# Kernel tuning notes

Hardware: AMD Instinct MI355X
Metric: run time of the kernel (lower is better)

Reference implementation:

```python
import jax, jax.numpy as jnp
import numpy as np

D_MODEL = 768
N_HEAD = 12
D_FF = 3072
SEQ = 2048
BSZ = 4
EPS = 1e-5


def _linear_params(key, d_in, d_out):
    k1, k2 = jax.random.split(key)
    bound = 1.0 / np.sqrt(d_in)
    W = jax.random.uniform(k1, (d_in, d_out), jnp.float32, -bound, bound)
    b = jax.random.uniform(k2, (d_out,), jnp.float32, -bound, bound)
    return W, b


def setup_inputs() -> dict:
    key = jax.random.key(0)
    ks = jax.random.split(key, 8)
    src = jax.random.normal(ks[0], (SEQ, BSZ, D_MODEL), jnp.float32)
    Wq, bq = _linear_params(ks[1], D_MODEL, D_MODEL)
    Wk, bk = _linear_params(ks[2], D_MODEL, D_MODEL)
    Wv, bv = _linear_params(ks[3], D_MODEL, D_MODEL)
    Wo, bo = _linear_params(ks[4], D_MODEL, D_MODEL)
    W1, b1 = _linear_params(ks[5], D_MODEL, D_FF)
    W2, b2 = _linear_params(ks[6], D_FF, D_MODEL)
    g1 = jnp.ones((D_MODEL,), jnp.float32)
    be1 = jnp.zeros((D_MODEL,), jnp.float32)
    g2 = jnp.ones((D_MODEL,), jnp.float32)
    be2 = jnp.zeros((D_MODEL,), jnp.float32)
    return dict(src=src, Wq=Wq, bq=bq, Wk=Wk, bk=bk, Wv=Wv, bv=bv,
                Wo=Wo, bo=bo, W1=W1, b1=b1, W2=W2, b2=b2,
                g1=g1, be1=be1, g2=g2, be2=be2)


def _layer_norm(x, g, b):
    mu = jnp.mean(x, axis=-1, keepdims=True)
    var = jnp.mean(jnp.square(x - mu), axis=-1, keepdims=True)
    return (x - mu) * jax.lax.rsqrt(var + EPS) * g + b


def reference(src, Wq, bq, Wk, bk, Wv, bv, Wo, bo, W1, b1, W2, b2, g1, be1, g2, be2):
    L, B, D = src.shape
    H = N_HEAD
    hd = D // H
    # in-projection: (L,B,D) -> (B*H, L, hd)
    def split_heads(x):
        return x.reshape(L, B * H, hd).transpose(1, 0, 2)
    q = split_heads(src @ Wq + bq)
    k = split_heads(src @ Wk + bk)
    v = split_heads(src @ Wv + bv)
    # NOTE: original code applies NO 1/sqrt(head_dim) scaling
    scores = jnp.einsum('bqd,bkd->bqk', q, k)  # (B*H, L, L)
    attn = jax.nn.softmax(scores, axis=-1)
    attn_out = jnp.einsum('bqk,bkd->bqd', attn, v)  # (B*H, L, hd)
    # out-projection
    attn_out = attn_out.transpose(1, 0, 2).reshape(L, B, D)
    src2 = attn_out @ Wo + bo
    x = _layer_norm(src + src2, g1, be1)
    ff = jax.nn.gelu(x @ W1 + b1, approximate=False) @ W2 + b2
    return _layer_norm(x + ff, g2, be2)
```

## Files before the change

kernel.cpp:

```cpp
#include <hip/hip_runtime.h>
#include <math.h>

#define D_MODEL 768
#define N_HEAD  12
#define HD      64
#define D_FF    3072
#define SEQ     2048
#define BSZ     4
#define NROWS   (SEQ * BSZ)

typedef unsigned short u16;
typedef __attribute__((ext_vector_type(8))) short short8;
typedef __attribute__((ext_vector_type(4))) float float4v;

enum { FLAG_GELU = 1 };

__device__ __forceinline__ float gelu_exact(float x) {
    return 0.5f * x * (1.0f + erff(x * 0.70710678118654752440f));
}
__device__ __forceinline__ u16 f2b(float f) {
    unsigned u = __builtin_bit_cast(unsigned, f);
    return (u16)((u + 0x7fffu + ((u >> 16) & 1u)) >> 16);
}
__device__ __forceinline__ float b2f(u16 x) {
    return __builtin_bit_cast(float, (unsigned)x << 16);
}
__device__ __forceinline__ void gll16(const u16* g, u16* l) {
    __builtin_amdgcn_global_load_lds(
        (const __attribute__((address_space(1))) unsigned*)g,
        (__attribute__((address_space(3))) unsigned*)l, 16, 0, 0);
}

__global__ __launch_bounds__(256) void gemm_bt(
    const u16* __restrict__ A, int lda,
    const u16* __restrict__ Bt, int ldb,
    const float* __restrict__ bias,
    const float* __restrict__ residf, const u16* __restrict__ residb, int ldr,
    float* __restrict__ Cf, u16* __restrict__ Cb, int ldc,
    int K, int flags)
{
    __shared__ u16 Ab[128 * 32];
    __shared__ u16 Bb[128 * 32];

    const int tid  = threadIdx.x;
    const int lane = tid & 63, wv = tid >> 6;
    const int row0 = blockIdx.x * 128, col0 = blockIdx.y * 128;
    const int mw = (wv & 1) * 64, nw = (wv >> 1) * 64;
    const int fr = lane & 15, fk = (lane >> 4) * 8;

    float4v acc[4][4];
    #pragma unroll
    for (int i = 0; i < 4; ++i)
        #pragma unroll
        for (int j = 0; j < 4; ++j)
            acc[i][j] = float4v{0.f, 0.f, 0.f, 0.f};

    for (int k0 = 0; k0 < K; k0 += 32) {
        __syncthreads();
        #pragma unroll
        for (int i = 0; i < 2; ++i) {
            const int cid = i * 256 + wv * 64 + lane;
            const int r = cid >> 2, ch = (cid & 3) * 8;
            gll16(A  + (size_t)(row0 + r) * lda + k0 + ch, Ab + (size_t)cid * 8);
            gll16(Bt + (size_t)(col0 + r) * ldb + k0 + ch, Bb + (size_t)cid * 8);
        }
        __syncthreads();

        short8 af[4], bfr[4];
        #pragma unroll
        for (int t = 0; t < 4; ++t) {
            af[t]  = *(const short8*)&Ab[(mw + t * 16 + fr) * 32 + fk];
            bfr[t] = *(const short8*)&Bb[(nw + t * 16 + fr) * 32 + fk];
        }
        #pragma unroll
        for (int mt = 0; mt < 4; ++mt)
            #pragma unroll
            for (int nt = 0; nt < 4; ++nt)
                acc[mt][nt] = __builtin_amdgcn_mfma_f32_16x16x32_bf16(
                    af[mt], bfr[nt], acc[mt][nt], 0, 0, 0);
    }

    #pragma unroll
    for (int mt = 0; mt < 4; ++mt)
        #pragma unroll
        for (int nt = 0; nt < 4; ++nt)
            #pragma unroll
            for (int r = 0; r < 4; ++r) {
                const int row = row0 + mw + mt * 16 + (lane >> 4) * 4 + r;
                const int col = col0 + nw + nt * 16 + fr;
                float v = acc[mt][nt][r];
                if (bias)              v += bias[col];
                if (flags & FLAG_GELU) v = gelu_exact(v);
                if (residf)            v += residf[(size_t)row * ldr + col];
                if (residb)            v += b2f(residb[(size_t)row * ldr + col]);
                if (Cf) Cf[(size_t)row * ldc + col] = v;
                if (Cb) Cb[(size_t)row * ldc + col] = f2b(v);
            }
}

__global__ __launch_bounds__(256) void vt_kernel(
    const u16* __restrict__ qkv, u16* __restrict__ vt)
{
    __shared__ u16 t[64][72];
    const int tid = threadIdx.x;
    const int bh = blockIdx.y, b = bh / N_HEAD, h = bh % N_HEAD;
    const int l0 = blockIdx.x * 64;
    #pragma unroll
    for (int p = 0; p < 2; ++p) {
        const int idx = p * 256 + tid;
        const int lr = idx >> 3, c8 = (idx & 7) * 8;
        *(short8*)&t[lr][c8] = *(const short8*)
            &qkv[((size_t)(l0 + lr) * BSZ + b) * 2304 + 1536 + h * 64 + c8];
    }
    __syncthreads();
    #pragma unroll
    for (int p = 0; p < 2; ++p) {
        const int idx = p * 256 + tid;
        const int dr = idx >> 3, l8 = (idx & 7) * 8;
        short8 vv;
        #pragma unroll
        for (int j = 0; j < 8; ++j) vv[j] = (short)t[l8 + j][dr];
        *(short8*)&vt[((size_t)(bh * 64 + dr)) * SEQ + l0 + l8] = vv;
    }
}

__global__ __launch_bounds__(256) void attn_kernel(
    const u16* __restrict__ qkv,
    const u16* __restrict__ vt,
    u16* __restrict__ o)
{
    __shared__ u16 Kt[64 * 64];
    __shared__ u16 Vt[64 * 64];
    __shared__ u16 PQ[128 * 72];

    const int tid  = threadIdx.x;
    const int lane = tid & 63, wv = tid >> 6;
    const int fr = lane & 15, hi = lane >> 4;
    const int bh = blockIdx.y, b = bh / N_HEAD, h = bh % N_HEAD;
    const int q0 = blockIdx.x * 128;

    #pragma unroll
    for (int i = 0; i < 4; ++i) {
        const int cid = i * 256 + wv * 64 + lane;
        const int r = cid >> 3, c = cid & 7;
        gll16(qkv + ((size_t)(q0 + r) * BSZ + b) * 2304 + h * 64 + ((c ^ (r & 7)) * 8),
              PQ + (size_t)cid * 8);
    }
    __syncthreads();
    short8 qf[2][2];
    #pragma unroll
    for (int mt = 0; mt < 2; ++mt) {
        const int row = wv * 32 + mt * 16 + fr;
        #pragma unroll
        for (int kb = 0; kb < 2; ++kb)
            qf[mt][kb] = *(const short8*)&PQ[row * 64 + (((kb << 2) + hi) ^ (fr & 7)) * 8];
    }

    const short8 ones = {(short)0x3F80, (short)0x3F80, (short)0x3F80, (short)0x3F80,
                         (short)0x3F80, (short)0x3F80, (short)0x3F80, (short)0x3F80};
    float4v oacc[2][4], ls[2];
    #pragma unroll
    for (int mt = 0; mt < 2; ++mt) {
        ls[mt] = float4v{0.f, 0.f, 0.f, 0.f};
        #pragma unroll
        for (int nt = 0; nt < 4; ++nt) oacc[mt][nt] = float4v{0.f, 0.f, 0.f, 0.f};
    }

    for (int kt = 0; kt < SEQ; kt += 64) {
        __syncthreads();
        #pragma unroll
        for (int i = 0; i < 2; ++i) {
            const int cid = i * 256 + wv * 64 + lane;
            const int r = cid >> 3, c = cid & 7;
            const int cs = (c ^ (r & 7)) * 8;
            gll16(qkv + ((size_t)(kt + r) * BSZ + b) * 2304 + 768 + h * 64 + cs,
                  Kt + (size_t)cid * 8);
            gll16(vt + (size_t)(bh * 64 + r) * SEQ + kt + cs,
                  Vt + (size_t)cid * 8);
        }
        __syncthreads();

        float4v s[2][4];
        #pragma unroll
        for (int mt = 0; mt < 2; ++mt)
            #pragma unroll
            for (int nt = 0; nt < 4; ++nt) s[mt][nt] = float4v{0.f, 0.f, 0.f, 0.f};
        #pragma unroll
        for (int kb = 0; kb < 2; ++kb) {
            short8 kfr[4];
            #pragma unroll
            for (int nt = 0; nt < 4; ++nt)
                kfr[nt] = *(const short8*)&Kt[(nt * 16 + fr) * 64 + (((kb << 2) + hi) ^ (fr & 7)) * 8];
            #pragma unroll
            for (int mt = 0; mt < 2; ++mt)
                #pragma unroll
                for (int nt = 0; nt < 4; ++nt)
                    s[mt][nt] = __builtin_amdgcn_mfma_f32_16x16x32_bf16(
                        qf[mt][kb], kfr[nt], s[mt][nt], 0, 0, 0);
        }

        #pragma unroll
        for (int mt = 0; mt < 2; ++mt)
            #pragma unroll
            for (int nt = 0; nt < 4; ++nt)
                #pragma unroll
                for (int r = 0; r < 4; ++r)
                    PQ[(wv * 32 + mt * 16 + hi * 4 + r) * 72 + nt * 16 + fr]
                        = f2b(__expf(s[mt][nt][r] - 16.0f));
        __syncthreads();

        #pragma unroll
        for (int kb = 0; kb < 2; ++kb) {
            short8 pf[2], vfr[4];
            #pragma unroll
            for (int mt = 0; mt < 2; ++mt)
                pf[mt] = *(const short8*)&PQ[(wv * 32 + mt * 16 + fr) * 72 + kb * 32 + hi * 8];
            #pragma unroll
            for (int nt = 0; nt < 4; ++nt)
                vfr[nt] = *(const short8*)&Vt[(nt * 16 + fr) * 64 + (((kb << 2) + hi) ^ (fr & 7)) * 8];
            #pragma unroll
            for (int mt = 0; mt < 2; ++mt) {
                ls[mt] = __builtin_amdgcn_mfma_f32_16x16x32_bf16(pf[mt], ones, ls[mt], 0, 0, 0);
                #pragma unroll
                for (int nt = 0; nt < 4; ++nt)
                    oacc[mt][nt] = __builtin_amdgcn_mfma_f32_16x16x32_bf16(
                        pf[mt], vfr[nt], oacc[mt][nt], 0, 0, 0);
            }
        }
    }

    #pragma unroll
    for (int mt = 0; mt < 2; ++mt)
        #pragma unroll
        for (int r = 0; r < 4; ++r) {
            const int qr = wv * 32 + mt * 16 + hi * 4 + r;
            const float linv = 1.0f / ls[mt][r];
            #pragma unroll
            for (int nt = 0; nt < 4; ++nt)
                o[((size_t)(q0 + qr) * BSZ + b) * D_MODEL + h * 64 + nt * 16 + fr]
                    = f2b(oacc[mt][nt][r] * linv);
        }
}

__global__ __launch_bounds__(256) void ln_kernel(
    const float* __restrict__ x, float* __restrict__ outf, u16* __restrict__ outb,
    const float* __restrict__ g, const float* __restrict__ be)
{
    const int row = blockIdx.x;
    const int tid = threadIdx.x;
    const float* xr = x + (size_t)row * D_MODEL;
    float v[3];
    float s = 0.0f, sq = 0.0f;
    #pragma unroll
    for (int j = 0; j < 3; ++j) {
        v[j] = xr[tid + 256 * j];
        s  += v[j];
        sq += v[j] * v[j];
    }
    #pragma unroll
    for (int off = 32; off > 0; off >>= 1) {
        s  += __shfl_down(s, off);
        sq += __shfl_down(sq, off);
    }
    __shared__ float ws_[8], wq_[8];
    if ((tid & 63) == 0) { ws_[tid >> 6] = s; wq_[tid >> 6] = sq; }
    __syncthreads();
    if (tid == 0) {
        float S = 0.0f, Q = 0.0f;
        #pragma unroll
        for (int w = 0; w < 4; ++w) { S += ws_[w]; Q += wq_[w]; }
        ws_[4] = S; wq_[4] = Q;
    }
    __syncthreads();
    const float mu   = ws_[4] * (1.0f / D_MODEL);
    const float var  = wq_[4] * (1.0f / D_MODEL) - mu * mu;
    const float rstd = rsqrtf(var + 1e-5f);
    #pragma unroll
    for (int j = 0; j < 3; ++j) {
        const int c = tid + 256 * j;
        const float y = (v[j] - mu) * rstd * g[c] + be[c];
        if (outf) outf[(size_t)row * D_MODEL + c] = y;
        if (outb) outb[(size_t)row * D_MODEL + c] = f2b(y);
    }
}

__global__ __launch_bounds__(256) void transpose_bf(
    const float* __restrict__ in, u16* __restrict__ out, int R, int Cn)
{
    __shared__ float t[32][33];
    const int c0 = blockIdx.x * 32, r0 = blockIdx.y * 32;
    const int tx = threadIdx.x & 31, ty = threadIdx.x >> 5;
    #pragma unroll
    for (int i = 0; i < 4; ++i)
        t[ty + i * 8][tx] = in[(size_t)(r0 + ty + i * 8) * Cn + c0 + tx];
    __syncthreads();
    #pragma unroll
    for (int i = 0; i < 4; ++i)
        out[(size_t)(c0 + ty + i * 8) * R + r0 + tx] = f2b(t[tx][ty + i * 8]);
}

__global__ __launch_bounds__(256) void conv_bf(
    const float* __restrict__ in, u16* __restrict__ out, int n4)
{
    const int i = blockIdx.x * 256 + threadIdx.x;
    if (i < n4) {
        const float4 vv = ((const float4*)in)[i];
        uint2 pk;
        pk.x = (unsigned)f2b(vv.x) | ((unsigned)f2b(vv.y) << 16);
        pk.y = (unsigned)f2b(vv.z) | ((unsigned)f2b(vv.w) << 16);
        ((uint2*)out)[i] = pk;
    }
}

__global__ __launch_bounds__(256) void pack_bias(
    const float* __restrict__ bq, const float* __restrict__ bk,
    const float* __restrict__ bv, float* __restrict__ dst)
{
    const int i = blockIdx.x * 256 + threadIdx.x;
    if (i < 2304)
        dst[i] = (i < 768) ? bq[i] : (i < 1536) ? bk[i - 768] : bv[i - 1536];
}

extern "C" void kernel_launch(void* const* d_in, const int* in_sizes, int n_in,
                              void* d_out, int out_size, void* d_ws, size_t ws_size,
                              hipStream_t stream)
{
    (void)in_sizes; (void)n_in; (void)out_size; (void)ws_size;
    const float* src = (const float*)d_in[0];
    const float* Wq  = (const float*)d_in[1];
    const float* bq  = (const float*)d_in[2];
    const float* Wk  = (const float*)d_in[3];
    const float* bk  = (const float*)d_in[4];
    const float* Wv  = (const float*)d_in[5];
    const float* bv  = (const float*)d_in[6];
    const float* Wo  = (const float*)d_in[7];
    const float* bo  = (const float*)d_in[8];
    const float* W1  = (const float*)d_in[9];
    const float* b1  = (const float*)d_in[10];
    const float* W2  = (const float*)d_in[11];
    const float* b2  = (const float*)d_in[12];
    const float* g1  = (const float*)d_in[13];
    const float* be1 = (const float*)d_in[14];
    const float* g2  = (const float*)d_in[15];
    const float* be2 = (const float*)d_in[16];
    float* out = (float*)d_out;

    char* w = (char*)d_ws;
    u16* WqkvT = (u16*)w; w += (size_t)2304 * 768 * 2;
    u16* WoT   = (u16*)w; w += (size_t)768 * 768 * 2;
    u16* W1T   = (u16*)w; w += (size_t)D_FF * 768 * 2;
    u16* W2T   = (u16*)w; w += (size_t)768 * D_FF * 2;
    float* bqkv = (float*)w; w += 2304 * 4 + 64;
    char* A0 = w; w += (size_t)NROWS * 768 * 2;
    char* A1 = w; w += (size_t)NROWS * 2304 * 2;
    char* A2 = w; w += (size_t)NROWS * 768 * 2;
    u16*   srcb  = (u16*)A0;
    u16*   vtb   = (u16*)A0;
    u16*   qkvb  = (u16*)A1;
    float* sum   = (float*)A1;
    u16*   attnb = (u16*)A2;
    u16*   x1b   = (u16*)A2;
    u16*   hb    = (u16*)A0;

    const dim3 blk(256);

    transpose_bf<<<dim3(24, 24), blk, 0, stream>>>(Wq, WqkvT,                 768, 768);
    transpose_bf<<<dim3(24, 24), blk, 0, stream>>>(Wk, WqkvT + 768 * 768,     768, 768);
    transpose_bf<<<dim3(24, 24), blk, 0, stream>>>(Wv, WqkvT + 2 * 768 * 768, 768, 768);
    transpose_bf<<<dim3(24, 24), blk, 0, stream>>>(Wo, WoT, 768, 768);
    transpose_bf<<<dim3(96, 24), blk, 0, stream>>>(W1, W1T, 768, 3072);
    transpose_bf<<<dim3(24, 96), blk, 0, stream>>>(W2, W2T, 3072, 768);
    pack_bias<<<dim3(9), blk, 0, stream>>>(bq, bk, bv, bqkv);
    conv_bf<<<dim3(NROWS * 768 / 4 / 256), blk, 0, stream>>>(src, srcb, NROWS * 768 / 4);

    gemm_bt<<<dim3(64, 18), blk, 0, stream>>>(srcb, 768, WqkvT, 768, bqkv,
        nullptr, nullptr, 0, nullptr, qkvb, 2304, 768, 0);

    vt_kernel<<<dim3(32, 48), blk, 0, stream>>>(qkvb, vtb);
    attn_kernel<<<dim3(SEQ / 128, BSZ * N_HEAD), blk, 0, stream>>>(qkvb, vtb, attnb);

    gemm_bt<<<dim3(64, 6), blk, 0, stream>>>(attnb, 768, WoT, 768, bo,
        src, nullptr, 768, sum, nullptr, 768, 768, 0);
    ln_kernel<<<NROWS, blk, 0, stream>>>(sum, nullptr, x1b, g1, be1);

    gemm_bt<<<dim3(64, 24), blk, 0, stream>>>(x1b, 768, W1T, 768, b1,
        nullptr, nullptr, 0, nullptr, hb, 3072, 768, FLAG_GELU);
    gemm_bt<<<dim3(64, 6), blk, 0, stream>>>(hb, 3072, W2T, 3072, b2,
        nullptr, x1b, 768, out, nullptr, 768, 3072, 0);

    ln_kernel<<<NROWS, blk, 0, stream>>>(out, out, nullptr, g2, be2);
}
```

Baseline: 569.4 us.

## Double-buffer GEMM and attention LDS tiles and split-K the narrow GEMMs

Gives the GEMM and attention kernels two LDS buffers each, so the next K/V or K tile is loaded asynchronously while the current one is computed, and one barrier per iteration is removed. The two N=768 GEMMs (out-projection and FFN down-projection) launch with split-K of 2 over gridDim.z and accumulate into memset-zeroed fp32 outputs with atomicAdd, which doubles the block count from 384 to 768 on a large-CU GPU. This adds memset launches and atomic traffic, and makes the fp32 summation order nondeterministic. Removing the barrier between the P write and the P read in attention depends on each wave reading only its own rows of PQ.

```diff
diff --git a/kernel.cpp b/kernel.cpp
--- a/kernel.cpp
+++ b/kernel.cpp
@@ -13,7 +13,7 @@
 typedef __attribute__((ext_vector_type(8))) short short8;
 typedef __attribute__((ext_vector_type(4))) float float4v;
 
-enum { FLAG_GELU = 1 };
+enum { FLAG_GELU = 1, FLAG_ATOMIC = 2 };
 
 __device__ __forceinline__ float gelu_exact(float x) {
     return 0.5f * x * (1.0f + erff(x * 0.70710678118654752440f));
@@ -39,8 +39,8 @@
     float* __restrict__ Cf, u16* __restrict__ Cb, int ldc,
     int K, int flags)
 {
-    __shared__ u16 Ab[128 * 32];
-    __shared__ u16 Bb[128 * 32];
+    __shared__ u16 Ab[2][128 * 32];
+    __shared__ u16 Bb[2][128 * 32];
 
     const int tid  = threadIdx.x;
     const int lane = tid & 63, wv = tid >> 6;
@@ -48,29 +48,39 @@
     const int mw = (wv & 1) * 64, nw = (wv >> 1) * 64;
     const int fr = lane & 15, fk = (lane >> 4) * 8;
 
-    float4v acc[4][4];
-    #pragma unroll
-    for (int i = 0; i < 4; ++i)
-        #pragma unroll
-        for (int j = 0; j < 4; ++j)
-            acc[i][j] = float4v{0.f, 0.f, 0.f, 0.f};
-
-    for (int k0 = 0; k0 < K; k0 += 32) {
-        __syncthreads();
+    int kBeg = 0, kChunk = K;
+    if (gridDim.z > 1) { kChunk = K / gridDim.z; kBeg = blockIdx.z * kChunk; }
+    const bool primary = (blockIdx.z == 0);
+    const int nIter = kChunk >> 5;
+
+    auto stage = [&](int buf, int k0) {
         #pragma unroll
         for (int i = 0; i < 2; ++i) {
             const int cid = i * 256 + wv * 64 + lane;
             const int r = cid >> 2, ch = (cid & 3) * 8;
-            gll16(A  + (size_t)(row0 + r) * lda + k0 + ch, Ab + (size_t)cid * 8);
-            gll16(Bt + (size_t)(col0 + r) * ldb + k0 + ch, Bb + (size_t)cid * 8);
-        }
+            gll16(A  + (size_t)(row0 + r) * lda + k0 + ch, Ab[buf] + (size_t)cid * 8);
+            gll16(Bt + (size_t)(col0 + r) * ldb + k0 + ch, Bb[buf] + (size_t)cid * 8);
+        }
+    };
+
+    float4v acc[4][4];
+    #pragma unroll
+    for (int i = 0; i < 4; ++i)
+        #pragma unroll
+        for (int j = 0; j < 4; ++j)
+            acc[i][j] = float4v{0.f, 0.f, 0.f, 0.f};
+
+    stage(0, kBeg);
+    for (int it = 0; it < nIter; ++it) {
+        const int cur = it & 1;
         __syncthreads();
+        if (it + 1 < nIter) stage(cur ^ 1, kBeg + (it + 1) * 32);
 
         short8 af[4], bfr[4];
         #pragma unroll
         for (int t = 0; t < 4; ++t) {
-            af[t]  = *(const short8*)&Ab[(mw + t * 16 + fr) * 32 + fk];
-            bfr[t] = *(const short8*)&Bb[(nw + t * 16 + fr) * 32 + fk];
+            af[t]  = *(const short8*)&Ab[cur][(mw + t * 16 + fr) * 32 + fk];
+            bfr[t] = *(const short8*)&Bb[cur][(nw + t * 16 + fr) * 32 + fk];
         }
         #pragma unroll
         for (int mt = 0; mt < 4; ++mt)
@@ -89,12 +99,18 @@
                 const int row = row0 + mw + mt * 16 + (lane >> 4) * 4 + r;
                 const int col = col0 + nw + nt * 16 + fr;
                 float v = acc[mt][nt][r];
-                if (bias)              v += bias[col];
-                if (flags & FLAG_GELU) v = gelu_exact(v);
-                if (residf)            v += residf[(size_t)row * ldr + col];
-                if (residb)            v += b2f(residb[(size_t)row * ldr + col]);
-                if (Cf) Cf[(size_t)row * ldc + col] = v;
-                if (Cb) Cb[(size_t)row * ldc + col] = f2b(v);
+                if (primary) {
+                    if (bias)              v += bias[col];
+                    if (flags & FLAG_GELU) v = gelu_exact(v);
+                    if (residf)            v += residf[(size_t)row * ldr + col];
+                    if (residb)            v += b2f(residb[(size_t)row * ldr + col]);
+                }
+                if (flags & FLAG_ATOMIC) {
+                    atomicAdd(&Cf[(size_t)row * ldc + col], v);
+                } else {
+                    if (Cf) Cf[(size_t)row * ldc + col] = v;
+                    if (Cb) Cb[(size_t)row * ldc + col] = f2b(v);
+                }
             }
 }
 
@@ -129,8 +145,8 @@
     const u16* __restrict__ vt,
     u16* __restrict__ o)
 {
-    __shared__ u16 Kt[64 * 64];
-    __shared__ u16 Vt[64 * 64];
+    __shared__ u16 Kt[2][64 * 64];
+    __shared__ u16 Vt[2][64 * 64];
     __shared__ u16 PQ[128 * 72];
 
     const int tid  = threadIdx.x;
@@ -139,6 +155,19 @@
     const int bh = blockIdx.y, b = bh / N_HEAD, h = bh % N_HEAD;
     const int q0 = blockIdx.x * 128;
 
+    auto stageKV = [&](int buf, int kt) {
+        #pragma unroll
+        for (int i = 0; i < 2; ++i) {
+            const int cid = i * 256 + wv * 64 + lane;
+            const int r = cid >> 3, c = cid & 7;
+            const int cs = (c ^ (r & 7)) * 8;
+            gll16(qkv + ((size_t)(kt + r) * BSZ + b) * 2304 + 768 + h * 64 + cs,
+                  Kt[buf] + (size_t)cid * 8);
+            gll16(vt + (size_t)(bh * 64 + r) * SEQ + kt + cs,
+                  Vt[buf] + (size_t)cid * 8);
+        }
+    };
+
     #pragma unroll
     for (int i = 0; i < 4; ++i) {
         const int cid = i * 256 + wv * 64 + lane;
@@ -146,7 +175,9 @@
         gll16(qkv + ((size_t)(q0 + r) * BSZ + b) * 2304 + h * 64 + ((c ^ (r & 7)) * 8),
               PQ + (size_t)cid * 8);
     }
+    stageKV(0, 0);
     __syncthreads();
+
     short8 qf[2][2];
     #pragma unroll
     for (int mt = 0; mt < 2; ++mt) {
@@ -166,19 +197,10 @@
         for (int nt = 0; nt < 4; ++nt) oacc[mt][nt] = float4v{0.f, 0.f, 0.f, 0.f};
     }
 
-    for (int kt = 0; kt < SEQ; kt += 64) {
+    for (int it = 0; it < SEQ / 64; ++it) {
+        const int cur = it & 1;
         __syncthreads();
-        #pragma unroll
-        for (int i = 0; i < 2; ++i) {
-            const int cid = i * 256 + wv * 64 + lane;
-            const int r = cid >> 3, c = cid & 7;
-            const int cs = (c ^ (r & 7)) * 8;
-            gll16(qkv + ((size_t)(kt + r) * BSZ + b) * 2304 + 768 + h * 64 + cs,
-                  Kt + (size_t)cid * 8);
-            gll16(vt + (size_t)(bh * 64 + r) * SEQ + kt + cs,
-                  Vt + (size_t)cid * 8);
-        }
-        __syncthreads();
+        if (it + 1 < SEQ / 64) stageKV(cur ^ 1, (it + 1) * 64);
 
         float4v s[2][4];
         #pragma unroll
@@ -190,7 +212,7 @@
             short8 kfr[4];
             #pragma unroll
             for (int nt = 0; nt < 4; ++nt)
-                kfr[nt] = *(const short8*)&Kt[(nt * 16 + fr) * 64 + (((kb << 2) + hi) ^ (fr & 7)) * 8];
+                kfr[nt] = *(const short8*)&Kt[cur][(nt * 16 + fr) * 64 + (((kb << 2) + hi) ^ (fr & 7)) * 8];
             #pragma unroll
             for (int mt = 0; mt < 2; ++mt)
                 #pragma unroll
@@ -207,7 +229,6 @@
                 for (int r = 0; r < 4; ++r)
                     PQ[(wv * 32 + mt * 16 + hi * 4 + r) * 72 + nt * 16 + fr]
                         = f2b(__expf(s[mt][nt][r] - 16.0f));
-        __syncthreads();
 
         #pragma unroll
         for (int kb = 0; kb < 2; ++kb) {
@@ -217,7 +238,7 @@
                 pf[mt] = *(const short8*)&PQ[(wv * 32 + mt * 16 + fr) * 72 + kb * 32 + hi * 8];
             #pragma unroll
             for (int nt = 0; nt < 4; ++nt)
-                vfr[nt] = *(const short8*)&Vt[(nt * 16 + fr) * 64 + (((kb << 2) + hi) ^ (fr & 7)) * 8];
+                vfr[nt] = *(const short8*)&Vt[cur][(nt * 16 + fr) * 64 + (((kb << 2) + hi) ^ (fr & 7)) * 8];
             #pragma unroll
             for (int mt = 0; mt < 2; ++mt) {
                 ls[mt] = __builtin_amdgcn_mfma_f32_16x16x32_bf16(pf[mt], ones, ls[mt], 0, 0, 0);
@@ -379,14 +400,16 @@
     vt_kernel<<<dim3(32, 48), blk, 0, stream>>>(qkvb, vtb);
     attn_kernel<<<dim3(SEQ / 128, BSZ * N_HEAD), blk, 0, stream>>>(qkvb, vtb, attnb);
 
-    gemm_bt<<<dim3(64, 6), blk, 0, stream>>>(attnb, 768, WoT, 768, bo,
-        src, nullptr, 768, sum, nullptr, 768, 768, 0);
+    hipMemsetAsync(sum, 0, (size_t)NROWS * 768 * 4, stream);
+    gemm_bt<<<dim3(64, 6, 2), blk, 0, stream>>>(attnb, 768, WoT, 768, bo,
+        src, nullptr, 768, sum, nullptr, 768, 768, FLAG_ATOMIC);
     ln_kernel<<<NROWS, blk, 0, stream>>>(sum, nullptr, x1b, g1, be1);
 
     gemm_bt<<<dim3(64, 24), blk, 0, stream>>>(x1b, 768, W1T, 768, b1,
         nullptr, nullptr, 0, nullptr, hb, 3072, 768, FLAG_GELU);
-    gemm_bt<<<dim3(64, 6), blk, 0, stream>>>(hb, 3072, W2T, 3072, b2,
-        nullptr, x1b, 768, out, nullptr, 768, 3072, 0);
+    hipMemsetAsync(out, 0, (size_t)NROWS * 768 * 4, stream);
+    gemm_bt<<<dim3(64, 6, 2), blk, 0, stream>>>(hb, 3072, W2T, 3072, b2,
+        nullptr, x1b, 768, out, nullptr, 768, 3072, FLAG_ATOMIC);
 
     ln_kernel<<<NROWS, blk, 0, stream>>>(out, out, nullptr, g2, be2);
 }
```

Result: slower. 592.7 us (+4.1%).
